# Kernel optimization log

Hardware: AMD Instinct MI355X
Metric: run time of the kernel (lower is better)

The kernel has to match this reference:

```python
import jax, jax.numpy as jnp
import numpy as np
from jax.scipy.special import logsumexp

EPS = 0.1
NUM_ITERS = 50
TOPO_MULT = 1.0


def _dist_cosine(x):
    # x: [N, D] -> pairwise cosine distance [N, N], clamped to >= 0
    norms = jnp.sqrt(jnp.clip(jnp.sum(x * x, axis=1, keepdims=True), 1e-8, None))
    xn = x / norms
    return jnp.clip(1.0 - xn @ xn.T, 0.0, None)


def _sinkhorn_log_domain(a, b, C):
    # a, b: [N, N] row-stochastic; C: [N, N]. Duals computed with no grad (detached).
    log_a = jnp.log(jnp.clip(a, 1e-8, None))
    log_b = jnp.log(jnp.clip(b, 1e-8, None))
    la = jax.lax.stop_gradient(log_a)
    lb = jax.lax.stop_gradient(log_b)
    lC = jax.lax.stop_gradient(-C / EPS)[None]  # [1, N, N]

    def body(i, fg):
        f, g = fg
        g = EPS * lb - EPS * logsumexp(f[:, :, None] + lC, axis=1)
        f = EPS * la - EPS * logsumexp(lC + g[:, None, :], axis=2)
        return (f, g)

    f0 = jnp.zeros_like(a)
    f, g = jax.lax.fori_loop(0, NUM_ITERS, body, (f0, f0))
    cost = jnp.sum(a * f, axis=1) + jnp.sum(b * g, axis=1)  # [N]
    return jnp.mean(cost)


def reference(x_original, x_reconstructed, z_latent, log_sigma_lat, log_var_recon, log_var_topo):
    recon_loss = jnp.mean((x_reconstructed - x_original) ** 2)

    D_orig = _dist_cosine(x_original)   # [N, N]
    D_latent = _dist_cosine(z_latent)   # [N, N]

    sigma_orig = jnp.median(D_orig)
    sigma_orig = jnp.where(sigma_orig == 0, jnp.asarray(1e-6, D_orig.dtype), sigma_orig)
    sigma_lat = jax.nn.softplus(log_sigma_lat) + 1e-6  # [1]

    S_orig = jnp.exp(-D_orig ** 2 / (2.0 * sigma_orig ** 2))
    S_lat = jnp.exp(-D_latent ** 2 / (2.0 * sigma_lat ** 2))

    N = S_orig.shape[0]
    mask = 1.0 - jnp.eye(N, dtype=S_orig.dtype)
    S_orig = S_orig * mask
    S_lat = S_lat * mask

    P_orig = S_orig / jnp.clip(jnp.sum(S_orig, axis=1, keepdims=True), 1e-8, None)
    P_lat = S_lat / jnp.clip(jnp.sum(S_lat, axis=1, keepdims=True), 1e-8, None)

    C = D_orig
    ot_orig_lat = _sinkhorn_log_domain(P_orig, P_lat, C)
    ot_lat_lat = _sinkhorn_log_domain(P_lat, P_lat, C)
    ot_orig_orig = _sinkhorn_log_domain(P_orig, P_orig, C)

    topo_loss = jnp.clip(ot_orig_lat - 0.5 * ot_lat_lat - 0.5 * ot_orig_orig, 0.0, None)
    topo_loss = topo_loss * TOPO_MULT

    prec_r = jnp.exp(-log_var_recon)  # [1]
    prec_t = jnp.exp(-log_var_topo)   # [1]
    total_loss = (0.5 * prec_r * recon_loss + 0.5 * log_var_recon
                  + 0.5 * prec_t * topo_loss + 0.5 * log_var_topo)  # [1]
    return (total_loss, recon_loss, topo_loss)


def setup_inputs() -> dict:
    key = jax.random.key(0)
    k1, k2, k3 = jax.random.split(key, 3)
    N, D, DL = 256, 4096, 256
    return {
        "x_original": jax.random.normal(k1, (N, D), dtype=jnp.float32),
        "x_reconstructed": jax.random.normal(k2, (N, D), dtype=jnp.float32),
        "z_latent": jax.random.normal(k3, (N, DL), dtype=jnp.float32),
        "log_sigma_lat": jnp.zeros((1,), dtype=jnp.float32),
        "log_var_recon": jnp.zeros((1,), dtype=jnp.float32),
        "log_var_topo": jnp.zeros((1,), dtype=jnp.float32),
    }
```

## Files before the change

### kernel.cpp

```cpp
#include <hip/hip_runtime.h>
#include <hip/hip_fp16.h>

#define EPS 0.1f
#define SINK_ITERS 50
#define KSCALE_LN 9.0109133472f
#define USTRIDE 272

typedef _Float16 f16;
typedef _Float16 f16x4 __attribute__((ext_vector_type(4)));
typedef _Float16 f16x8 __attribute__((ext_vector_type(8)));
typedef float f32x4 __attribute__((ext_vector_type(4)));

#define PIN_U4(v) asm volatile("" : "+v"(v.x), "+v"(v.y), "+v"(v.z), "+v"(v.w))

__device__ __forceinline__ float wave_red_sum(float v) {
    #pragma unroll
    for (int o = 32; o; o >>= 1) v += __shfl_xor(v, o, 64);
    return v;
}

__device__ __forceinline__ float sel4(int q, float a, float b, float c, float d) {
    float ab = (q & 1) ? b : a;
    float cd = (q & 1) ? d : c;
    return (q & 2) ? cd : ab;
}

__global__ __launch_bounds__(256) void k_pre(const float4* __restrict__ xo,
                                             const float4* __restrict__ xr,
                                             const float4* __restrict__ z,
                                             f16x4* __restrict__ xh,
                                             f16x4* __restrict__ zh,
                                             float* __restrict__ acc) {
    __shared__ float red[4];
    int b = blockIdx.x, t = threadIdx.x;
    if (b < 512) {
        int tid = b * 256 + t;
        float s = 0.f;
        for (int i = tid; i < 262144; i += 512 * 256) {
            float4 a = xo[i], r = xr[i];
            float d0 = r.x - a.x, d1 = r.y - a.y, d2 = r.z - a.z, d3 = r.w - a.w;
            s = fmaf(d0, d0, s); s = fmaf(d1, d1, s);
            s = fmaf(d2, d2, s); s = fmaf(d3, d3, s);
        }
        s = wave_red_sum(s);
        if ((t & 63) == 0) red[t >> 6] = s;
        __syncthreads();
        if (t == 0) atomicAdd(acc + 3, red[0] + red[1] + red[2] + red[3]);
    } else {
        int row = b - 512;
        const float4* src; f16x4* dst; int c4;
        if (row < 256) { src = xo + (size_t)row * 1024; dst = xh + (size_t)row * 1024; c4 = 1024; }
        else { src = z + (size_t)(row - 256) * 64; dst = zh + (size_t)(row - 256) * 64; c4 = 64; }
        float s = 0.f;
        for (int i = t; i < c4; i += 256) {
            float4 v = src[i];
            s = fmaf(v.x, v.x, s); s = fmaf(v.y, v.y, s);
            s = fmaf(v.z, v.z, s); s = fmaf(v.w, v.w, s);
        }
        s = wave_red_sum(s);
        if ((t & 63) == 0) red[t >> 6] = s;
        __syncthreads();
        float tot = red[0] + red[1] + red[2] + red[3];
        float rn = 1.f / sqrtf(fmaxf(tot, 1e-8f));
        for (int i = t; i < c4; i += 256) {
            float4 v = src[i];
            f16x4 h;
            h[0] = (f16)(v.x * rn); h[1] = (f16)(v.y * rn);
            h[2] = (f16)(v.z * rn); h[3] = (f16)(v.w * rn);
            dst[i] = h;
        }
    }
}

__global__ __launch_bounds__(256) void k_gemm_f16(const uint4* __restrict__ xh,
                                                  const uint4* __restrict__ zh,
                                                  float* __restrict__ part,
                                                  float* __restrict__ part2) {
    __shared__ __align__(16) f16 Ai[64 * 40], Bj[64 * 40];
    int zb = blockIdx.z;
    const uint4* X; int lda8, k0, nchunk; float* out;
    if (zb < 16) { X = xh; lda8 = 512; k0 = zb * 256; nchunk = 8; out = part + (size_t)zb * 65536; }
    else { X = zh; lda8 = 32; k0 = (zb - 16) * 64; nchunk = 2; out = part2 + (size_t)(zb - 16) * 65536; }
    int i0 = blockIdx.x * 64, j0 = blockIdx.y * 64;
    int t = threadIdx.x, lane = t & 63, wv = t >> 6;
    int m16 = lane & 15, quad = lane >> 4;
    int r = t >> 2, ko = (t & 3) * 8;
    f32x4 acc[4] = {};
    for (int ch = 0; ch < nchunk; ch++) {
        int kb8 = (k0 + ch * 32) >> 3;
        uint4 va = X[(size_t)(i0 + r) * lda8 + kb8 + (t & 3)];
        uint4 vb = X[(size_t)(j0 + r) * lda8 + kb8 + (t & 3)];
        __syncthreads();
        *(uint4*)&Ai[r * 40 + ko] = va;
        *(uint4*)&Bj[r * 40 + ko] = vb;
        __syncthreads();
        f16x8 a = *(const f16x8*)&Ai[(wv * 16 + m16) * 40 + quad * 8];
        #pragma unroll
        for (int st = 0; st < 4; st++) {
            f16x8 bfr = *(const f16x8*)&Bj[(st * 16 + m16) * 40 + quad * 8];
            acc[st] = __builtin_amdgcn_mfma_f32_16x16x32_f16(a, bfr, acc[st], 0, 0, 0);
        }
    }
    #pragma unroll
    for (int st = 0; st < 4; st++)
        #pragma unroll
        for (int reg = 0; reg < 4; reg++)
            out[(i0 + wv * 16 + quad * 4 + reg) * 256 + j0 + st * 16 + m16] = acc[st][reg];
}

__global__ __launch_bounds__(256) void k_reduce_do(const float* __restrict__ part,
                                                   float* __restrict__ Do) {
    int e = blockIdx.x * 256 + threadIdx.x;
    float s = 0.f;
    for (int sl = 0; sl < 16; sl++) s += part[(size_t)sl * 65536 + e];
    Do[e] = fmaxf(1.f - s, 0.f);
}

__device__ __forceinline__ int med_bin(float v) {
    int b = (int)(v * 4096.f);
    if (v < (float)b * (1.f / 4096.f)) b--;
    else if (v >= (float)(b + 1) * (1.f / 4096.f)) b++;
    if (b < 0) b = 0;
    if (b > 8191) b = 8191;
    return b;
}

__global__ __launch_bounds__(1024) void k_median(const float* __restrict__ D,
                                                 float* __restrict__ out_sigma) {
    __shared__ int hist[8192];
    __shared__ int redc[16];
    __shared__ int sh_bin[2];
    __shared__ int sh_tot;
    int t = threadIdx.x;
    unsigned r[64];
    #pragma unroll
    for (int i = 0; i < 64; i++) r[i] = __float_as_uint(D[t + i * 1024]);
    #pragma unroll
    for (int j = 0; j < 8; j++) hist[t + j * 1024] = 0;
    __syncthreads();
    #pragma unroll
    for (int i = 0; i < 64; i++)
        atomicAdd(&hist[med_bin(__uint_as_float(r[i]))], 1);
    __syncthreads();
    int s8 = 0;
    #pragma unroll
    for (int j = 0; j < 8; j++) s8 += hist[t * 8 + j];
    int inc = s8;
    #pragma unroll
    for (int o = 1; o < 64; o <<= 1) {
        int vv = __shfl_up(inc, o, 64);
        if ((t & 63) >= o) inc += vv;
    }
    if ((t & 63) == 63) redc[t >> 6] = inc;
    __syncthreads();
    int woff = 0;
    for (int wv = 0; wv < (t >> 6); wv++) woff += redc[wv];
    int excl = woff + inc - s8;
    for (int sel = 0; sel < 2; sel++) {
        int k = 32767 + sel;
        if (excl <= k && k < excl + s8) {
            int cum = excl, bfound = 8191;
            bool found = false;
            for (int j = 0; j < 8; j++) {
                int hc = hist[t * 8 + j];
                if (!found) {
                    if (cum + hc > k) { bfound = t * 8 + j; found = true; }
                    else cum += hc;
                }
            }
            sh_bin[sel] = bfound;
        }
    }
    __syncthreads();
    unsigned res[2];
    for (int sel = 0; sel < 2; sel++) {
        int k = 32767 + sel;
        int b = sh_bin[sel];
        unsigned lo = __float_as_uint((float)b * (1.f / 4096.f));
        unsigned hi = __float_as_uint((float)(b + 1) * (1.f / 4096.f));
        while (hi - lo > 1u) {
            unsigned mid = (lo + hi) >> 1;
            int c = 0;
            #pragma unroll
            for (int i = 0; i < 64; i++) c += (r[i] < mid) ? 1 : 0;
            #pragma unroll
            for (int o = 32; o; o >>= 1) c += __shfl_xor(c, o, 64);
            if ((t & 63) == 0) redc[t >> 6] = c;
            __syncthreads();
            if (t == 0) {
                int tot = 0;
                for (int wv = 0; wv < 16; wv++) tot += redc[wv];
                sh_tot = tot;
            }
            __syncthreads();
            if (sh_tot <= k) lo = mid; else hi = mid;
        }
        res[sel] = lo;
    }
    if (t == 0)
        out_sigma[0] = 0.5f * (__uint_as_float(res[0]) + __uint_as_float(res[1]));
}

__global__ __launch_bounds__(256) void k_prep(const float* __restrict__ Do,
                                              const float* __restrict__ part2,
                                              const float* __restrict__ wsacc,
                                              const float* __restrict__ lsl,
                                              float* __restrict__ Po, float* __restrict__ Pl,
                                              float* __restrict__ ELo, float* __restrict__ ELl,
                                              f16* __restrict__ Kh) {
    __shared__ float red[8];
    int i = blockIdx.x, j = threadIdx.x;
    int e = i * 256 + j;
    float sig_o = wsacc[4];
    if (sig_o == 0.f) sig_o = 1e-6f;
    float x = lsl[0];
    float sp = (x > 20.f) ? x : log1pf(__expf(x));
    float sig_l = sp + 1e-6f;
    float i2o = 1.f / (2.f * sig_o * sig_o);
    float i2l = 1.f / (2.f * sig_l * sig_l);
    float d_o = Do[e];
    float sD = part2[e] + part2[65536 + e] + part2[131072 + e] + part2[196608 + e];
    float d_l = fmaxf(1.f - sD, 0.f);
    float so = (i == j) ? 0.f : __expf(-d_o * d_o * i2o);
    float sl = (i == j) ? 0.f : __expf(-d_l * d_l * i2l);
    float wso = wave_red_sum(so);
    float wsl = wave_red_sum(sl);
    if ((j & 63) == 0) { red[j >> 6] = wso; red[4 + (j >> 6)] = wsl; }
    __syncthreads();
    float sum_o = red[0] + red[1] + red[2] + red[3];
    float sum_l = red[4] + red[5] + red[6] + red[7];
    float po = so / fmaxf(sum_o, 1e-8f);
    float pl = sl / fmaxf(sum_l, 1e-8f);
    Po[e] = po;
    Pl[e] = pl;
    ELo[e] = EPS * __logf(fmaxf(po, 1e-8f));
    ELl[e] = EPS * __logf(fmaxf(pl, 1e-8f));
    float kv = __expf(-d_o * (1.f / EPS) + KSCALE_LN);
    Kh[(((i >> 3) * 256 + j) << 3) + (i & 7)] = (f16)kv;
}

__global__ __launch_bounds__(256, 1) void k_sinkhorn(const float* __restrict__ Po,
                                                     const float* __restrict__ Pl,
                                                     const float* __restrict__ ELo,
                                                     const float* __restrict__ ELl,
                                                     const uint4* __restrict__ Kq,
                                                     float* __restrict__ wsacc) {
    __shared__ __align__(16) f16 U[2][4 * USTRIDE];
    __shared__ float CW[4][4];
    int t = threadIdx.x;
    int lane = t & 63, wv = t >> 6;
    int m16 = lane & 15, quad = lane >> 4;
    int w = blockIdx.x;
    int s = w >> 6;
    int ibase = (w & 63) * 4;
    int colbase = wv * 64;
    int c_lane = colbase + quad * 16 + m16;

    uint4 bf[4][8];
    #pragma unroll
    for (int ct = 0; ct < 4; ct++)
        #pragma unroll
        for (int kc = 0; kc < 8; kc++)
            bf[ct][kc] = Kq[(kc * 4 + quad) * 256 + colbase + ct * 16 + m16];
    #pragma unroll
    for (int ct = 0; ct < 4; ct++)
        #pragma unroll
        for (int kc = 0; kc < 8; kc++) PIN_U4(bf[ct][kc]);

    const float* ELa_b = (s == 1 ? ELl : ELo);
    const float* ELb_b = (s == 2 ? ELo : ELl);
    float ef[4], eg[4], Ef[4], Eg[4];
    #pragma unroll
    for (int reg = 0; reg < 4; reg++) {
        int i = ibase + reg;
        ef[reg] = ELa_b[i * 256 + c_lane] + EPS * KSCALE_LN;
        eg[reg] = ELb_b[i * 256 + c_lane] + EPS * KSCALE_LN;
        Ef[reg] = __expf(ef[reg]);
        Eg[reg] = __expf(eg[reg]);
    }

    if (t < 136)
        *(uint4*)&U[0][t * 8] =
            make_uint4(0x3C003C00u, 0x3C003C00u, 0x3C003C00u, 0x3C003C00u);
    __syncthreads();

    float zf[4], zg[4];
    for (int it = 0; it < 2 * SINK_ITERS; it++) {
        const f16* ub = &U[it & 1][0];
        f16* un = &U[(it + 1) & 1][0];
        f16x8 a[8];
        #pragma unroll
        for (int kc = 0; kc < 8; kc++)
            a[kc] = *(const f16x8*)&ub[(m16 & 3) * USTRIDE + kc * 32 + quad * 8];
        f32x4 accA[4] = {{0.f,0.f,0.f,0.f},{0.f,0.f,0.f,0.f},{0.f,0.f,0.f,0.f},{0.f,0.f,0.f,0.f}};
        f32x4 accB[4] = {{0.f,0.f,0.f,0.f},{0.f,0.f,0.f,0.f},{0.f,0.f,0.f,0.f},{0.f,0.f,0.f,0.f}};
        #pragma unroll
        for (int kc = 0; kc < 4; kc++)
            #pragma unroll
            for (int ct = 0; ct < 4; ct++)
                accA[ct] = __builtin_amdgcn_mfma_f32_16x16x32_f16(
                    a[kc], __builtin_bit_cast(f16x8, bf[ct][kc]), accA[ct], 0, 0, 0);
        #pragma unroll
        for (int kc = 4; kc < 8; kc++)
            #pragma unroll
            for (int ct = 0; ct < 4; ct++)
                accB[ct] = __builtin_amdgcn_mfma_f32_16x16x32_f16(
                    a[kc], __builtin_bit_cast(f16x8, bf[ct][kc]), accB[ct], 0, 0, 0);
        float zsum[4];
        #pragma unroll
        for (int reg = 0; reg < 4; reg++) {
            float zA = sel4(quad, accA[0][reg], accA[1][reg], accA[2][reg], accA[3][reg]);
            float zB = sel4(quad, accB[0][reg], accB[1][reg], accB[2][reg], accB[3][reg]);
            zsum[reg] = zA + zB;
        }
        if (it == 2 * SINK_ITERS - 2) {
            #pragma unroll
            for (int reg = 0; reg < 4; reg++) zg[reg] = zsum[reg];
        }
        if (it == 2 * SINK_ITERS - 1) {
            #pragma unroll
            for (int reg = 0; reg < 4; reg++) zf[reg] = zsum[reg];
        }
        bool fstep = (it & 1);
        #pragma unroll
        for (int reg = 0; reg < 4; reg++) {
            float E = fstep ? Ef[reg] : Eg[reg];
            float p = __expf(-EPS * __logf(zsum[reg]));
            un[reg * USTRIDE + c_lane] = (f16)(E * p);
        }
        __syncthreads();
    }

    const float* PaB = (s == 1 ? Pl : Po);
    const float* PbB = (s == 2 ? Po : Pl);
    float cs[4];
    #pragma unroll
    for (int reg = 0; reg < 4; reg++) {
        int i = ibase + reg;
        float dfv = ef[reg] - EPS * __logf(zf[reg]);
        float dgv = eg[reg] - EPS * __logf(zg[reg]);
        cs[reg] = PaB[i * 256 + c_lane] * dfv + PbB[i * 256 + c_lane] * dgv;
    }
    #pragma unroll
    for (int reg = 0; reg < 4; reg++) cs[reg] = wave_red_sum(cs[reg]);
    if (lane == 0) {
        #pragma unroll
        for (int reg = 0; reg < 4; reg++) CW[wv][reg] = cs[reg];
    }
    __syncthreads();
    if (t == 0) {
        float v = 0.f;
        for (int w2 = 0; w2 < 4; w2++)
            v += CW[w2][0] + CW[w2][1] + CW[w2][2] + CW[w2][3];
        atomicAdd(&wsacc[s], v);
    }
}

__global__ void k_final(const float* __restrict__ wsacc, const float* __restrict__ lvr_p,
                        const float* __restrict__ lvt_p, float* __restrict__ out) {
    float recon = wsacc[3] * (1.f / (256.f * 4096.f));
    float ot0 = wsacc[0] * (1.f / 256.f);
    float ot1 = wsacc[1] * (1.f / 256.f);
    float ot2 = wsacc[2] * (1.f / 256.f);
    float topo = ot0 - 0.5f * ot1 - 0.5f * ot2;
    topo = topo > 0.f ? topo : 0.f;
    float lvr = lvr_p[0], lvt = lvt_p[0];
    out[0] = 0.5f * __expf(-lvr) * recon + 0.5f * lvr +
             0.5f * __expf(-lvt) * topo + 0.5f * lvt;
    out[1] = recon;
    out[2] = topo;
}

extern "C" void kernel_launch(void* const* d_in, const int* in_sizes, int n_in,
                              void* d_out, int out_size, void* d_ws, size_t ws_size,
                              hipStream_t stream) {
    const float* xo = (const float*)d_in[0];
    const float* xr = (const float*)d_in[1];
    const float* z  = (const float*)d_in[2];
    const float* lsl = (const float*)d_in[3];
    const float* lvr = (const float*)d_in[4];
    const float* lvt = (const float*)d_in[5];
    float* out = (float*)d_out;
    float* ws = (float*)d_ws;

    float* acc = ws;
    float* xh  = ws + 64;
    float* zh  = xh + 524288;
    float* Do  = zh + 32768;
    float* Po  = Do + 65536;
    float* Pl  = Po + 65536;
    float* ELo = Pl + 65536;
    float* ELl = ELo + 65536;
    float* Kh  = ELl + 65536;
    float* part = Kh + 32768;
    float* part2 = Po;

    (void)hipMemsetAsync(acc, 0, 64, stream);
    k_pre<<<1024, 256, 0, stream>>>((const float4*)xo, (const float4*)xr, (const float4*)z,
                                    (f16x4*)xh, (f16x4*)zh, acc);
    k_gemm_f16<<<dim3(4, 4, 20), 256, 0, stream>>>((const uint4*)xh, (const uint4*)zh,
                                                   part, part2);
    k_reduce_do<<<256, 256, 0, stream>>>(part, Do);
    k_median<<<1, 1024, 0, stream>>>(Do, acc + 4);
    k_prep<<<256, 256, 0, stream>>>(Do, part2, acc, lsl, Po, Pl, ELo, ELl, (f16*)Kh);
    k_sinkhorn<<<192, 256, 0, stream>>>(Po, Pl, ELo, ELl, (const uint4*)Kh, acc);
    k_final<<<1, 1, 0, stream>>>(acc, lvr, lvt, out);
}
```

Baseline: 206.3 us.

## Split Sinkhorn work to one row per block across 768 blocks

Each Sinkhorn block now handles a single row (problem instance) instead of four, and the grid grows from 192 to 768 blocks so more CUs run the serial 100-step loop concurrently. The MFMA still runs on the full 16-row tile, but only one row of the result is used. Every block reloads the full K matrix into registers, which multiplies global/L2 traffic by four. The MFMA section is also wrapped in s_setprio raises. With launch_bounds(256,1) and a large register footprint, 768 blocks exceed the 256 CUs, so blocks may run in several waves.

```diff
diff --git a/kernel.cpp b/kernel.cpp
--- a/kernel.cpp
+++ b/kernel.cpp
@@ -4,7 +4,6 @@
 #define EPS 0.1f
 #define SINK_ITERS 50
 #define KSCALE_LN 9.0109133472f
-#define USTRIDE 272
 
 typedef _Float16 f16;
 typedef _Float16 f16x4 __attribute__((ext_vector_type(4)));
@@ -245,14 +244,14 @@
                                                      const float* __restrict__ ELl,
                                                      const uint4* __restrict__ Kq,
                                                      float* __restrict__ wsacc) {
-    __shared__ __align__(16) f16 U[2][4 * USTRIDE];
-    __shared__ float CW[4][4];
+    __shared__ __align__(16) f16 U[2][272];
+    __shared__ float CW[4];
     int t = threadIdx.x;
     int lane = t & 63, wv = t >> 6;
     int m16 = lane & 15, quad = lane >> 4;
     int w = blockIdx.x;
-    int s = w >> 6;
-    int ibase = (w & 63) * 4;
+    int s = w >> 8;
+    int i = w & 255;
     int colbase = wv * 64;
     int c_lane = colbase + quad * 16 + m16;
 
@@ -269,31 +268,27 @@
 
     const float* ELa_b = (s == 1 ? ELl : ELo);
     const float* ELb_b = (s == 2 ? ELo : ELl);
-    float ef[4], eg[4], Ef[4], Eg[4];
-    #pragma unroll
-    for (int reg = 0; reg < 4; reg++) {
-        int i = ibase + reg;
-        ef[reg] = ELa_b[i * 256 + c_lane] + EPS * KSCALE_LN;
-        eg[reg] = ELb_b[i * 256 + c_lane] + EPS * KSCALE_LN;
-        Ef[reg] = __expf(ef[reg]);
-        Eg[reg] = __expf(eg[reg]);
-    }
-
-    if (t < 136)
+    float ef_ = ELa_b[i * 256 + c_lane] + EPS * KSCALE_LN;
+    float eg_ = ELb_b[i * 256 + c_lane] + EPS * KSCALE_LN;
+    float Ef_ = __expf(ef_);
+    float Eg_ = __expf(eg_);
+
+    if (t < 34)
         *(uint4*)&U[0][t * 8] =
             make_uint4(0x3C003C00u, 0x3C003C00u, 0x3C003C00u, 0x3C003C00u);
     __syncthreads();
 
-    float zf[4], zg[4];
+    float zf_ = 1.f, zg_ = 1.f;
     for (int it = 0; it < 2 * SINK_ITERS; it++) {
         const f16* ub = &U[it & 1][0];
         f16* un = &U[(it + 1) & 1][0];
         f16x8 a[8];
         #pragma unroll
         for (int kc = 0; kc < 8; kc++)
-            a[kc] = *(const f16x8*)&ub[(m16 & 3) * USTRIDE + kc * 32 + quad * 8];
+            a[kc] = *(const f16x8*)&ub[kc * 32 + quad * 8];
         f32x4 accA[4] = {{0.f,0.f,0.f,0.f},{0.f,0.f,0.f,0.f},{0.f,0.f,0.f,0.f},{0.f,0.f,0.f,0.f}};
         f32x4 accB[4] = {{0.f,0.f,0.f,0.f},{0.f,0.f,0.f,0.f},{0.f,0.f,0.f,0.f},{0.f,0.f,0.f,0.f}};
+        __builtin_amdgcn_s_setprio(1);
         #pragma unroll
         for (int kc = 0; kc < 4; kc++)
             #pragma unroll
@@ -306,54 +301,27 @@
             for (int ct = 0; ct < 4; ct++)
                 accB[ct] = __builtin_amdgcn_mfma_f32_16x16x32_f16(
                     a[kc], __builtin_bit_cast(f16x8, bf[ct][kc]), accB[ct], 0, 0, 0);
-        float zsum[4];
-        #pragma unroll
-        for (int reg = 0; reg < 4; reg++) {
-            float zA = sel4(quad, accA[0][reg], accA[1][reg], accA[2][reg], accA[3][reg]);
-            float zB = sel4(quad, accB[0][reg], accB[1][reg], accB[2][reg], accB[3][reg]);
-            zsum[reg] = zA + zB;
-        }
-        if (it == 2 * SINK_ITERS - 2) {
-            #pragma unroll
-            for (int reg = 0; reg < 4; reg++) zg[reg] = zsum[reg];
-        }
-        if (it == 2 * SINK_ITERS - 1) {
-            #pragma unroll
-            for (int reg = 0; reg < 4; reg++) zf[reg] = zsum[reg];
-        }
-        bool fstep = (it & 1);
-        #pragma unroll
-        for (int reg = 0; reg < 4; reg++) {
-            float E = fstep ? Ef[reg] : Eg[reg];
-            float p = __expf(-EPS * __logf(zsum[reg]));
-            un[reg * USTRIDE + c_lane] = (f16)(E * p);
-        }
+        __builtin_amdgcn_s_setprio(0);
+        float zA = sel4(quad, accA[0][0], accA[1][0], accA[2][0], accA[3][0]);
+        float zB = sel4(quad, accB[0][0], accB[1][0], accB[2][0], accB[3][0]);
+        float zsum = zA + zB;
+        if (it == 2 * SINK_ITERS - 2) zg_ = zsum;
+        if (it == 2 * SINK_ITERS - 1) zf_ = zsum;
+        float E = (it & 1) ? Ef_ : Eg_;
+        un[c_lane] = (f16)(E * __expf(-EPS * __logf(zsum)));
         __syncthreads();
     }
 
     const float* PaB = (s == 1 ? Pl : Po);
     const float* PbB = (s == 2 ? Po : Pl);
-    float cs[4];
-    #pragma unroll
-    for (int reg = 0; reg < 4; reg++) {
-        int i = ibase + reg;
-        float dfv = ef[reg] - EPS * __logf(zf[reg]);
-        float dgv = eg[reg] - EPS * __logf(zg[reg]);
-        cs[reg] = PaB[i * 256 + c_lane] * dfv + PbB[i * 256 + c_lane] * dgv;
-    }
-    #pragma unroll
-    for (int reg = 0; reg < 4; reg++) cs[reg] = wave_red_sum(cs[reg]);
-    if (lane == 0) {
-        #pragma unroll
-        for (int reg = 0; reg < 4; reg++) CW[wv][reg] = cs[reg];
-    }
-    __syncthreads();
-    if (t == 0) {
-        float v = 0.f;
-        for (int w2 = 0; w2 < 4; w2++)
-            v += CW[w2][0] + CW[w2][1] + CW[w2][2] + CW[w2][3];
-        atomicAdd(&wsacc[s], v);
-    }
+    float dfv = ef_ - EPS * __logf(zf_);
+    float dgv = eg_ - EPS * __logf(zg_);
+    float cs = PaB[i * 256 + c_lane] * dfv + PbB[i * 256 + c_lane] * dgv;
+    cs = wave_red_sum(cs);
+    if (lane == 0) CW[wv] = cs;
+    __syncthreads();
+    if (t == 0)
+        atomicAdd(&wsacc[s], CW[0] + CW[1] + CW[2] + CW[3]);
 }
 
 __global__ void k_final(const float* __restrict__ wsacc, const float* __restrict__ lvr_p,
@@ -403,6 +371,6 @@
     k_reduce_do<<<256, 256, 0, stream>>>(part, Do);
     k_median<<<1, 1024, 0, stream>>>(Do, acc + 4);
     k_prep<<<256, 256, 0, stream>>>(Do, part2, acc, lsl, Po, Pl, ELo, ELl, (f16*)Kh);
-    k_sinkhorn<<<192, 256, 0, stream>>>(Po, Pl, ELo, ELl, (const uint4*)Kh, acc);
+    k_sinkhorn<<<768, 256, 0, stream>>>(Po, Pl, ELo, ELl, (const uint4*)Kh, acc);
     k_final<<<1, 1, 0, stream>>>(acc, lvr, lvt, out);
 }
```

Result: slower. 232.3 us (+12.6%).

## Process two independent 4-row groups per sinkhorn block, halving block count

Applied to the files above, without the earlier changes.

Each sinkhorn block now handles 8 rows as two independent 4-row groups, with separate LDS buffers and alternating phases, so the grid shrinks from 192 to 96 blocks. The aim is to halve the per-block cost of loading the register-resident K fragments and to run on fewer CUs. The cost is that each block does twice the serial MFMA and barrier work per iteration (two syncs instead of one), which could lengthen the critical path.

```diff
diff --git a/kernel.cpp b/kernel.cpp
--- a/kernel.cpp
+++ b/kernel.cpp
@@ -239,20 +239,55 @@
     Kh[(((i >> 3) * 256 + j) << 3) + (i & 7)] = (f16)kv;
 }
 
+__device__ __forceinline__ void sink_phase(const f16* __restrict__ ub, f16* __restrict__ un,
+                                           int arow, int quad, int c_lane,
+                                           const uint4 bf[4][8], bool fstep, int save,
+                                           const float* Ef, const float* Eg,
+                                           float* zf, float* zg) {
+    f16x8 a[8];
+    #pragma unroll
+    for (int kc = 0; kc < 8; kc++)
+        a[kc] = *(const f16x8*)&ub[arow * USTRIDE + kc * 32 + quad * 8];
+    f32x4 accA[4] = {{0.f,0.f,0.f,0.f},{0.f,0.f,0.f,0.f},{0.f,0.f,0.f,0.f},{0.f,0.f,0.f,0.f}};
+    f32x4 accB[4] = {{0.f,0.f,0.f,0.f},{0.f,0.f,0.f,0.f},{0.f,0.f,0.f,0.f},{0.f,0.f,0.f,0.f}};
+    #pragma unroll
+    for (int kc = 0; kc < 4; kc++)
+        #pragma unroll
+        for (int ct = 0; ct < 4; ct++)
+            accA[ct] = __builtin_amdgcn_mfma_f32_16x16x32_f16(
+                a[kc], __builtin_bit_cast(f16x8, bf[ct][kc]), accA[ct], 0, 0, 0);
+    #pragma unroll
+    for (int kc = 4; kc < 8; kc++)
+        #pragma unroll
+        for (int ct = 0; ct < 4; ct++)
+            accB[ct] = __builtin_amdgcn_mfma_f32_16x16x32_f16(
+                a[kc], __builtin_bit_cast(f16x8, bf[ct][kc]), accB[ct], 0, 0, 0);
+    #pragma unroll
+    for (int p = 0; p < 4; p++) {
+        float zA = sel4(quad, accA[0][p], accA[1][p], accA[2][p], accA[3][p]);
+        float zB = sel4(quad, accB[0][p], accB[1][p], accB[2][p], accB[3][p]);
+        float z = zA + zB;
+        if (save == 1) zg[p] = z;
+        if (save == 2) zf[p] = z;
+        float E = fstep ? Ef[p] : Eg[p];
+        un[p * USTRIDE + c_lane] = (f16)(E * __expf(-EPS * __logf(z)));
+    }
+}
+
 __global__ __launch_bounds__(256, 1) void k_sinkhorn(const float* __restrict__ Po,
                                                      const float* __restrict__ Pl,
                                                      const float* __restrict__ ELo,
                                                      const float* __restrict__ ELl,
                                                      const uint4* __restrict__ Kq,
                                                      float* __restrict__ wsacc) {
-    __shared__ __align__(16) f16 U[2][4 * USTRIDE];
-    __shared__ float CW[4][4];
+    __shared__ __align__(16) f16 U[2][2][4 * USTRIDE];
+    __shared__ float CW[4][8];
     int t = threadIdx.x;
     int lane = t & 63, wv = t >> 6;
     int m16 = lane & 15, quad = lane >> 4;
     int w = blockIdx.x;
-    int s = w >> 6;
-    int ibase = (w & 63) * 4;
+    int s = w >> 5;
+    int ibase = (w & 31) * 8;
     int colbase = wv * 64;
     int c_lane = colbase + quad * 16 + m16;
 
@@ -269,89 +304,59 @@
 
     const float* ELa_b = (s == 1 ? ELl : ELo);
     const float* ELb_b = (s == 2 ? ELo : ELl);
-    float ef[4], eg[4], Ef[4], Eg[4];
-    #pragma unroll
-    for (int reg = 0; reg < 4; reg++) {
-        int i = ibase + reg;
-        ef[reg] = ELa_b[i * 256 + c_lane] + EPS * KSCALE_LN;
-        eg[reg] = ELb_b[i * 256 + c_lane] + EPS * KSCALE_LN;
-        Ef[reg] = __expf(ef[reg]);
-        Eg[reg] = __expf(eg[reg]);
-    }
-
-    if (t < 136)
-        *(uint4*)&U[0][t * 8] =
+    float ef[8], eg[8], Ef[8], Eg[8];
+    #pragma unroll
+    for (int p = 0; p < 8; p++) {
+        int i = ibase + p;
+        ef[p] = ELa_b[i * 256 + c_lane] + EPS * KSCALE_LN;
+        eg[p] = ELb_b[i * 256 + c_lane] + EPS * KSCALE_LN;
+        Ef[p] = __expf(ef[p]);
+        Eg[p] = __expf(eg[p]);
+    }
+
+    for (int idx = t; idx < 272; idx += 256) {
+        int g = idx / 136, o = idx - g * 136;
+        *(uint4*)&U[g][0][o * 8] =
             make_uint4(0x3C003C00u, 0x3C003C00u, 0x3C003C00u, 0x3C003C00u);
-    __syncthreads();
-
-    float zf[4], zg[4];
+    }
+    __syncthreads();
+
+    int arow = m16 & 3;
+    float zf[8], zg[8];
     for (int it = 0; it < 2 * SINK_ITERS; it++) {
-        const f16* ub = &U[it & 1][0];
-        f16* un = &U[(it + 1) & 1][0];
-        f16x8 a[8];
-        #pragma unroll
-        for (int kc = 0; kc < 8; kc++)
-            a[kc] = *(const f16x8*)&ub[(m16 & 3) * USTRIDE + kc * 32 + quad * 8];
-        f32x4 accA[4] = {{0.f,0.f,0.f,0.f},{0.f,0.f,0.f,0.f},{0.f,0.f,0.f,0.f},{0.f,0.f,0.f,0.f}};
-        f32x4 accB[4] = {{0.f,0.f,0.f,0.f},{0.f,0.f,0.f,0.f},{0.f,0.f,0.f,0.f},{0.f,0.f,0.f,0.f}};
-        #pragma unroll
-        for (int kc = 0; kc < 4; kc++)
-            #pragma unroll
-            for (int ct = 0; ct < 4; ct++)
-                accA[ct] = __builtin_amdgcn_mfma_f32_16x16x32_f16(
-                    a[kc], __builtin_bit_cast(f16x8, bf[ct][kc]), accA[ct], 0, 0, 0);
-        #pragma unroll
-        for (int kc = 4; kc < 8; kc++)
-            #pragma unroll
-            for (int ct = 0; ct < 4; ct++)
-                accB[ct] = __builtin_amdgcn_mfma_f32_16x16x32_f16(
-                    a[kc], __builtin_bit_cast(f16x8, bf[ct][kc]), accB[ct], 0, 0, 0);
-        float zsum[4];
-        #pragma unroll
-        for (int reg = 0; reg < 4; reg++) {
-            float zA = sel4(quad, accA[0][reg], accA[1][reg], accA[2][reg], accA[3][reg]);
-            float zB = sel4(quad, accB[0][reg], accB[1][reg], accB[2][reg], accB[3][reg]);
-            zsum[reg] = zA + zB;
-        }
-        if (it == 2 * SINK_ITERS - 2) {
-            #pragma unroll
-            for (int reg = 0; reg < 4; reg++) zg[reg] = zsum[reg];
-        }
-        if (it == 2 * SINK_ITERS - 1) {
-            #pragma unroll
-            for (int reg = 0; reg < 4; reg++) zf[reg] = zsum[reg];
-        }
+        int cur = it & 1, nxt = cur ^ 1;
         bool fstep = (it & 1);
-        #pragma unroll
-        for (int reg = 0; reg < 4; reg++) {
-            float E = fstep ? Ef[reg] : Eg[reg];
-            float p = __expf(-EPS * __logf(zsum[reg]));
-            un[reg * USTRIDE + c_lane] = (f16)(E * p);
-        }
+        int save = (it == 2 * SINK_ITERS - 2) ? 1 : (it == 2 * SINK_ITERS - 1) ? 2 : 0;
+        sink_phase(&U[0][cur][0], &U[0][nxt][0], arow, quad, c_lane, bf,
+                   fstep, save, Ef, Eg, zf, zg);
+        __syncthreads();
+        sink_phase(&U[1][cur][0], &U[1][nxt][0], arow, quad, c_lane, bf,
+                   fstep, save, Ef + 4, Eg + 4, zf + 4, zg + 4);
         __syncthreads();
     }
 
     const float* PaB = (s == 1 ? Pl : Po);
     const float* PbB = (s == 2 ? Po : Pl);
-    float cs[4];
-    #pragma unroll
-    for (int reg = 0; reg < 4; reg++) {
-        int i = ibase + reg;
-        float dfv = ef[reg] - EPS * __logf(zf[reg]);
-        float dgv = eg[reg] - EPS * __logf(zg[reg]);
-        cs[reg] = PaB[i * 256 + c_lane] * dfv + PbB[i * 256 + c_lane] * dgv;
-    }
-    #pragma unroll
-    for (int reg = 0; reg < 4; reg++) cs[reg] = wave_red_sum(cs[reg]);
+    float cs[8];
+    #pragma unroll
+    for (int p = 0; p < 8; p++) {
+        int i = ibase + p;
+        float dfv = ef[p] - EPS * __logf(zf[p]);
+        float dgv = eg[p] - EPS * __logf(zg[p]);
+        cs[p] = PaB[i * 256 + c_lane] * dfv + PbB[i * 256 + c_lane] * dgv;
+    }
+    #pragma unroll
+    for (int p = 0; p < 8; p++) cs[p] = wave_red_sum(cs[p]);
     if (lane == 0) {
         #pragma unroll
-        for (int reg = 0; reg < 4; reg++) CW[wv][reg] = cs[reg];
+        for (int p = 0; p < 8; p++) CW[wv][p] = cs[p];
     }
     __syncthreads();
     if (t == 0) {
         float v = 0.f;
         for (int w2 = 0; w2 < 4; w2++)
-            v += CW[w2][0] + CW[w2][1] + CW[w2][2] + CW[w2][3];
+            #pragma unroll
+            for (int p = 0; p < 8; p++) v += CW[w2][p];
         atomicAdd(&wsacc[s], v);
     }
 }
@@ -403,6 +408,6 @@
     k_reduce_do<<<256, 256, 0, stream>>>(part, Do);
     k_median<<<1, 1024, 0, stream>>>(Do, acc + 4);
     k_prep<<<256, 256, 0, stream>>>(Do, part2, acc, lsl, Po, Pl, ELo, ELl, (f16*)Kh);
-    k_sinkhorn<<<192, 256, 0, stream>>>(Po, Pl, ELo, ELl, (const uint4*)Kh, acc);
+    k_sinkhorn<<<96, 256, 0, stream>>>(Po, Pl, ELo, ELl, (const uint4*)Kh, acc);
     k_final<<<1, 1, 0, stream>>>(acc, lvr, lvt, out);
 }
```

New measurement: 266.2 us. 1.29x slower.

## Replace median bisection with candidate-bin gather and rank selection

Applied to the files above, without the earlier changes.

The median kernel no longer bisects over float bit patterns with a block-wide count reduction and two barriers per step. It now gathers the values falling in the one or two histogram bins that hold the median into shared memory and finds the exact order statistics by an all-pairs rank count. This removes roughly two dozen barrier-synchronised passes over 64 registers per thread. In exchange it adds an O(C^2) rank loop, and the result is wrong if more than 6144 candidates land in those bins, because the buffer silently truncates.

```diff
diff --git a/kernel.cpp b/kernel.cpp
--- a/kernel.cpp
+++ b/kernel.cpp
@@ -125,80 +125,80 @@
     return b;
 }
 
+#define MED_CAP 6144
+
 __global__ __launch_bounds__(1024) void k_median(const float* __restrict__ D,
                                                  float* __restrict__ out_sigma) {
     __shared__ int hist[8192];
-    __shared__ int redc[16];
-    __shared__ int sh_bin[2];
-    __shared__ int sh_tot;
+    __shared__ float cand[MED_CAP];
+    __shared__ int scan_w[16];
+    __shared__ int s_cnt;
+    __shared__ int s_b[2], s_r[2];
+    __shared__ float s_out[2];
     int t = threadIdx.x;
-    unsigned r[64];
-    #pragma unroll
-    for (int i = 0; i < 64; i++) r[i] = __float_as_uint(D[t + i * 1024]);
+    float r[64];
+    #pragma unroll
+    for (int i = 0; i < 64; i++) r[i] = D[t + i * 1024];
     #pragma unroll
     for (int j = 0; j < 8; j++) hist[t + j * 1024] = 0;
+    if (t == 0) s_cnt = 0;
     __syncthreads();
     #pragma unroll
     for (int i = 0; i < 64; i++)
-        atomicAdd(&hist[med_bin(__uint_as_float(r[i]))], 1);
-    __syncthreads();
+        atomicAdd(&hist[med_bin(r[i])], 1);
+    __syncthreads();
+    int loc[8];
     int s8 = 0;
     #pragma unroll
-    for (int j = 0; j < 8; j++) s8 += hist[t * 8 + j];
+    for (int j = 0; j < 8; j++) { loc[j] = s8; s8 += hist[t * 8 + j]; }
     int inc = s8;
     #pragma unroll
     for (int o = 1; o < 64; o <<= 1) {
         int vv = __shfl_up(inc, o, 64);
         if ((t & 63) >= o) inc += vv;
     }
-    if ((t & 63) == 63) redc[t >> 6] = inc;
+    if ((t & 63) == 63) scan_w[t >> 6] = inc;
     __syncthreads();
     int woff = 0;
-    for (int wv = 0; wv < (t >> 6); wv++) woff += redc[wv];
-    int excl = woff + inc - s8;
+    for (int wv = 0; wv < (t >> 6); wv++) woff += scan_w[wv];
+    int base = woff + inc - s8;
     for (int sel = 0; sel < 2; sel++) {
         int k = 32767 + sel;
-        if (excl <= k && k < excl + s8) {
-            int cum = excl, bfound = 8191;
-            bool found = false;
+        if (base <= k && k < base + s8) {
+            #pragma unroll
             for (int j = 0; j < 8; j++) {
-                int hc = hist[t * 8 + j];
-                if (!found) {
-                    if (cum + hc > k) { bfound = t * 8 + j; found = true; }
-                    else cum += hc;
-                }
+                int lo = base + loc[j], hi = lo + hist[t * 8 + j];
+                if (lo <= k && k < hi) { s_b[sel] = t * 8 + j; s_r[sel] = k - lo; }
             }
-            sh_bin[sel] = bfound;
-        }
-    }
-    __syncthreads();
-    unsigned res[2];
-    for (int sel = 0; sel < 2; sel++) {
-        int k = 32767 + sel;
-        int b = sh_bin[sel];
-        unsigned lo = __float_as_uint((float)b * (1.f / 4096.f));
-        unsigned hi = __float_as_uint((float)(b + 1) * (1.f / 4096.f));
-        while (hi - lo > 1u) {
-            unsigned mid = (lo + hi) >> 1;
-            int c = 0;
-            #pragma unroll
-            for (int i = 0; i < 64; i++) c += (r[i] < mid) ? 1 : 0;
-            #pragma unroll
-            for (int o = 32; o; o >>= 1) c += __shfl_xor(c, o, 64);
-            if ((t & 63) == 0) redc[t >> 6] = c;
-            __syncthreads();
-            if (t == 0) {
-                int tot = 0;
-                for (int wv = 0; wv < 16; wv++) tot += redc[wv];
-                sh_tot = tot;
-            }
-            __syncthreads();
-            if (sh_tot <= k) lo = mid; else hi = mid;
-        }
-        res[sel] = lo;
-    }
+        }
+    }
+    __syncthreads();
+    int b0 = s_b[0], b1 = s_b[1];
+    #pragma unroll
+    for (int i = 0; i < 64; i++) {
+        int b = med_bin(r[i]);
+        if (b == b0 || b == b1) {
+            int idx = atomicAdd(&s_cnt, 1);
+            if (idx < MED_CAP) cand[idx] = r[i];
+        }
+    }
+    __syncthreads();
+    int C = s_cnt < MED_CAP ? s_cnt : MED_CAP;
+    int t0 = s_r[0];
+    int t1 = (b1 == b0) ? s_r[1] : (hist[b0] + s_r[1]);
+    for (int j = t; j < C; j += 1024) {
+        float vj = cand[j];
+        int rk = 0;
+        for (int i = 0; i < C; i++) {
+            float vi = cand[i];
+            rk += (vi < vj || (vi == vj && i < j)) ? 1 : 0;
+        }
+        if (rk == t0) s_out[0] = vj;
+        if (rk == t1) s_out[1] = vj;
+    }
+    __syncthreads();
     if (t == 0)
-        out_sigma[0] = 0.5f * (__uint_as_float(res[0]) + __uint_as_float(res[1]));
+        out_sigma[0] = 0.5f * (s_out[0] + s_out[1]);
 }
 
 __global__ __launch_bounds__(256) void k_prep(const float* __restrict__ Do,
```

Result: slower. 216.4 us (+4.9%).
